# Kernel tuning notes

Hardware: AMD Instinct MI355X
Metric: run time of the kernel (lower is better)

The kernel has to match this reference:

```python
import jax, jax.numpy as jnp
import numpy as np

B, T, D, V, L, HM = 4, 2048, 128, 64, 12, 512
EPS = 1e-5
SCALE = float(np.sqrt(D))


def setup_inputs() -> dict:
    key = jax.random.key(0)
    ks = jax.random.split(key, 12)
    s = 0.02
    x = jax.random.randint(ks[0], (B, T), 0, V)
    pos_emb = jax.random.normal(ks[1], (T, D), jnp.float32) * s
    # per-layer params stacked on leading L axis; Linear weights in torch (out,in) layout
    Wq = jax.random.normal(ks[2], (L, D, D), jnp.float32) * s
    Wk = jax.random.normal(ks[3], (L, D, D), jnp.float32) * s
    Wv = jax.random.normal(ks[4], (L, D, D), jnp.float32) * s
    ln1_g = jnp.ones((L, D), jnp.float32)
    ln1_b = jnp.zeros((L, D), jnp.float32)
    W1 = jax.random.normal(ks[5], (L, HM, D), jnp.float32) * s
    b1 = jnp.zeros((L, HM), jnp.float32)
    W2 = jax.random.normal(ks[6], (L, D, HM), jnp.float32) * s
    b2 = jnp.zeros((L, D), jnp.float32)
    ln2_g = jnp.ones((L, D), jnp.float32)
    ln2_b = jnp.zeros((L, D), jnp.float32)
    Wro = jax.random.normal(ks[7], (1, D), jnp.float32) * s
    bro = jnp.zeros((1,), jnp.float32)
    return dict(x=x, pos_emb=pos_emb, Wq=Wq, Wk=Wk, Wv=Wv, ln1_g=ln1_g, ln1_b=ln1_b,
                W1=W1, b1=b1, W2=W2, b2=b2, ln2_g=ln2_g, ln2_b=ln2_b, Wro=Wro, bro=bro)


def _layernorm(h, g, b):
    mu = jnp.mean(h, axis=-1, keepdims=True)
    var = jnp.mean(jnp.square(h - mu), axis=-1, keepdims=True)
    return (h - mu) * jax.lax.rsqrt(var + EPS) * g + b


def _token_embeddings(x):
    # -(c - x)^2 / 2 over class ids, zero-padded up to D
    ar = jnp.arange(V, dtype=jnp.float32)  # [V]
    leave = -jnp.square(ar - x[..., None].astype(jnp.float32)) * 0.5  # [B,T,V]
    return jnp.pad(leave, ((0, 0), (0, 0), (0, D - V)))  # [B,T,D]


def _forward(x, pos_emb, Wq, Wk, Wv, ln1_g, ln1_b, W1, b1, W2, b2, ln2_g, ln2_b, Wro, bro):
    H = _token_embeddings(x) + pos_emb[None]  # [B,T,D]

    def step(Hc, p):
        wq, wk, wv, g1, be1, w1, bb1, w2, bb2, g2, be2 = p
        H1 = _layernorm(Hc, g1, be1)
        q = H1 @ wq.T
        k = H1 @ wk.T
        v = H1 @ wv.T
        scores = jnp.einsum('bid,bjd->bij', q, k) / SCALE  # [B,T,T]
        attn = jax.nn.softmax(scores, axis=-1)
        Hc = Hc + jnp.einsum('bij,bjd->bid', attn, v)
        H2 = _layernorm(Hc, g2, be2)
        Hc = Hc + (jax.nn.gelu(H2 @ w1.T + bb1, approximate=False) @ w2.T + bb2)
        return Hc, None

    H, _ = jax.lax.scan(step, H, (Wq, Wk, Wv, ln1_g, ln1_b, W1, b1, W2, b2, ln2_g, ln2_b))
    pred = H @ Wro.T + bro  # [B,T,1]
    return pred[:, :, 0]


def reference(x, pos_emb, Wq, Wk, Wv, ln1_g, ln1_b, W1, b1, W2, b2, ln2_g, ln2_b, Wro, bro):
    return _forward(x, pos_emb, Wq, Wk, Wv, ln1_g, ln1_b, W1, b1, W2, b2, ln2_g, ln2_b, Wro, bro)
```

## Files before the change

kernel.cpp:

```cpp
#include <hip/hip_runtime.h>
#include <math.h>

#define D 128
#define T 2048
#define BATCH 4
#define HMID 512
#define NLAYER 12

#define KSPLIT 8
#define KPB (T / KSPLIT)
#define BK 64

#if defined(__has_builtin)
#if __has_builtin(__builtin_amdgcn_global_load_lds)
#define USE_GLL 1
#endif
#endif
#ifndef USE_GLL
#define USE_GLL 0
#endif

typedef unsigned short u16;
typedef __attribute__((ext_vector_type(8))) short bf16x8;
typedef __attribute__((ext_vector_type(16))) float f32x16;

__device__ inline u16 f2bf(float x) {
    unsigned u = __builtin_bit_cast(unsigned, x);
    return (u16)((u + 0x7FFFu + ((u >> 16) & 1u)) >> 16);
}
__device__ inline float bf2f(u16 v) {
    return __builtin_bit_cast(float, (unsigned)v << 16);
}
__device__ inline unsigned pkt(float a, float b) {
    return (__builtin_bit_cast(unsigned, a) >> 16) |
           (__builtin_bit_cast(unsigned, b) & 0xFFFF0000u);
}

__device__ inline void ln_stats32(const float (*Ct)[133], float* mu_s, float* rs_s, int tid) {
    const int q = tid >> 3, e8 = tid & 7;
    float s = 0.f;
#pragma unroll
    for (int c = 0; c < 16; c++) s += Ct[q][e8 * 16 + c];
    s += __shfl_xor(s, 1); s += __shfl_xor(s, 2); s += __shfl_xor(s, 4);
    float mu = s * (1.f / D);
    float s2 = 0.f;
#pragma unroll
    for (int c = 0; c < 16; c++) {
        float d0 = Ct[q][e8 * 16 + c] - mu;
        s2 += d0 * d0;
    }
    s2 += __shfl_xor(s2, 1); s2 += __shfl_xor(s2, 2); s2 += __shfl_xor(s2, 4);
    if (e8 == 0) { mu_s[q] = mu; rs_s[q] = rsqrtf(s2 * (1.f / D) + 1e-5f); }
}

__device__ inline void build_as(const float (*Ct)[133], const float* mu_s, const float* rs_s,
                                const float* __restrict__ g, const float* __restrict__ bb,
                                u16* As, int tid) {
    const int row = tid >> 3, e8 = tid & 7;
    const float mu = mu_s[row], rs = rs_s[row];
#pragma unroll
    for (int cc = 0; cc < 2; cc++) {
        int c = e8 * 2 + cc;
        u16 tmp[8];
#pragma unroll
        for (int j = 0; j < 8; j++) {
            int d = c * 8 + j;
            tmp[j] = f2bf((Ct[row][d] - mu) * rs * g[d] + bb[d]);
        }
        *(uint4*)&As[((size_t)c * 32 + (row ^ (c & 7))) * 8] = *(uint4*)tmp;
    }
}

__device__ inline void stage_w(const u16* __restrict__ W, int ldw, u16* Wst, int tid) {
#pragma unroll
    for (int i = 0; i < 8; i++) {
        int ci = tid + 256 * i;
        int row = ci >> 4, c = ci & 15;
        *(uint4*)&Wst[((size_t)c * 128 + (row ^ c)) * 8] =
            *(const uint4*)(W + (size_t)row * ldw + c * 8);
    }
}

__device__ inline f32x16 mm_32x128(const u16* As, const u16* Wst, int wv, int ql, int h) {
    f32x16 a;
#pragma unroll
    for (int r = 0; r < 16; r++) a[r] = 0.f;
#pragma unroll
    for (int s = 0; s < 8; s++) {
        int ch = 2 * s + h;
        bf16x8 af = *(const bf16x8*)&As[((size_t)ch * 32 + (ql ^ (ch & 7))) * 8];
        bf16x8 bf = *(const bf16x8*)&Wst[((size_t)ch * 128 + ((wv * 32 + ql) ^ ch)) * 8];
        a = __builtin_amdgcn_mfma_f32_32x32x16_bf16(af, bf, a, 0, 0, 0);
    }
    return a;
}

__device__ inline void qkv_phase(const u16* As, const u16* __restrict__ Wqkvl, u16* Wst,
                                 u16* __restrict__ qb, u16* __restrict__ kb,
                                 u16* __restrict__ vt, int m0, int tid) {
    const int wv = tid >> 6, l = tid & 63, h = l >> 5, ql = l & 31;
    const int bbk = m0 >> 11;
    const int tl0 = m0 & 2047;
#pragma unroll
    for (int sl = 0; sl < 3; sl++) {
        __syncthreads();
        stage_w(Wqkvl + (size_t)sl * 128 * D, D, Wst, tid);
        __syncthreads();
        f32x16 a = mm_32x128(As, Wst, wv, ql, h);
        const int n = wv * 32 + ql;
        if (sl == 2) {
            u16* dst = vt + (size_t)bbk * D * T + (size_t)n * T + tl0;
#pragma unroll
            for (int g = 0; g < 4; g++) {
                ushort4 o;
                o.x = f2bf(a[4 * g + 0]);
                o.y = f2bf(a[4 * g + 1]);
                o.z = f2bf(a[4 * g + 2]);
                o.w = f2bf(a[4 * g + 3]);
                *(ushort4*)(dst + 8 * g + 4 * h) = o;
            }
        } else {
            u16* dst = (sl == 0) ? qb : kb;
#pragma unroll
            for (int r = 0; r < 16; r++) {
                int row = (r & 3) + 8 * (r >> 2) + 4 * h;
                dst[(size_t)(m0 + row) * D + n] = f2bf(a[r]);
            }
        }
    }
}

__global__ __launch_bounds__(256) void conv_all(const float* __restrict__ Wq,
                                                const float* __restrict__ Wk,
                                                const float* __restrict__ Wv,
                                                const float* __restrict__ W1,
                                                const float* __restrict__ W2,
                                                u16* __restrict__ Wqkv,
                                                u16* __restrict__ W1b,
                                                u16* __restrict__ W2b, float qscale) {
    const int NQ = NLAYER * 3 * D * D;
    const int NW = NLAYER * HMID * D;
    int idx = blockIdx.x * 256 + threadIdx.x;
    if (idx < NQ) {
        int lN = idx / (3 * D * D);
        int rem = idx - lN * (3 * D * D);
        int s = rem >> 14;
        int off = rem & 16383;
        const float* src = (s == 0) ? Wq : ((s == 1) ? Wk : Wv);
        Wqkv[idx] = f2bf(src[lN * 16384 + off] * ((s == 0) ? qscale : 1.f));
    } else if (idx < NQ + NW) {
        W1b[idx - NQ] = f2bf(W1[idx - NQ]);
    } else if (idx < NQ + 2 * NW) {
        W2b[idx - NQ - NW] = f2bf(W2[idx - NQ - NW]);
    }
}

__global__ __launch_bounds__(256, 1) void embed_qkv(const int* __restrict__ x,
                                                    const float* __restrict__ pos,
                                                    const float* __restrict__ g1,
                                                    const float* __restrict__ b1g,
                                                    const u16* __restrict__ Wqkv0,
                                                    u16* __restrict__ qb, u16* __restrict__ kb,
                                                    u16* __restrict__ vt,
                                                    float* __restrict__ H) {
    __shared__ float Ct[32][133];
    __shared__ float mu_s[32], rs_s[32];
    __shared__ u16 As[16 * 32 * 8];
    __shared__ u16 Wst[16 * 128 * 8];
    const int tid = threadIdx.x;
    const int m0 = blockIdx.x * 32;
    {
        const int d = tid & 127, rr = tid >> 7;
#pragma unroll
        for (int i = 0; i < 16; i++) {
            int row = rr * 16 + i;
            int tok = m0 + row;
            int t = tok & (T - 1);
            float e = 0.f;
            if (d < 64) {
                float diff = (float)d - (float)x[tok];
                e = -0.5f * diff * diff;
            }
            float v = e + pos[(size_t)t * D + d];
            Ct[row][d] = v;
            H[(size_t)tok * D + d] = v;
        }
    }
    __syncthreads();
    ln_stats32(Ct, mu_s, rs_s, tid);
    __syncthreads();
    build_as(Ct, mu_s, rs_s, g1, b1g, As, tid);
    qkv_phase(As, Wqkv0, Wst, qb, kb, vt, m0, tid);
}

__global__ __launch_bounds__(256, 2) void attn_mfma(const u16* __restrict__ qg,
                                                    const u16* __restrict__ kg,
                                                    const u16* __restrict__ vtg,
                                                    u16* __restrict__ Op,
                                                    float* __restrict__ ml) {
    __shared__ u16 Ks[64 * 128];
    __shared__ u16 Vt[128 * 64];
    const int tid = threadIdx.x;
    const int w = tid >> 6;
    const int l = tid & 63;
    const int h = l >> 5;
    const int ql = l & 31;
    const int qblk = blockIdx.x;
    const int ks = blockIdx.y;
    const int b = qblk >> 4;

    const size_t qrow = (size_t)qblk * 128 + w * 32 + ql;
    bf16x8 qf[8];
#pragma unroll
    for (int c = 0; c < 8; c++)
        qf[c] = *(const bf16x8*)(qg + qrow * D + c * 16 + h * 8);

    f32x16 ot[4];
#pragma unroll
    for (int t = 0; t < 4; t++)
#pragma unroll
        for (int r = 0; r < 16; r++) ot[t][r] = 0.f;
    float l_run = 0.f;

    const size_t kgb = (size_t)b * T * D;
    const size_t vtb = (size_t)b * D * T;

    for (int kt = 0; kt < KPB / BK; kt++) {
        const int kbase = ks * KPB + kt * BK;
        __syncthreads();
#if USE_GLL
#pragma unroll
        for (int i = 0; i < 4; i++) {
            int s = w * 256 + i * 64 + l;
            int row = s >> 4, ch = (s & 15) ^ (row & 7);
            __builtin_amdgcn_global_load_lds(
                (const __attribute__((address_space(1))) void*)(kg + kgb + (size_t)(kbase + row) * D + ch * 8),
                (__attribute__((address_space(3))) void*)&Ks[(w * 256 + i * 64) * 8], 16, 0, 0);
        }
#pragma unroll
        for (int i = 0; i < 4; i++) {
            int s = w * 256 + i * 64 + l;
            int dd = s >> 3, ch = (s & 7) ^ (dd & 7);
            __builtin_amdgcn_global_load_lds(
                (const __attribute__((address_space(1))) void*)(vtg + vtb + (size_t)dd * T + kbase + ch * 8),
                (__attribute__((address_space(3))) void*)&Vt[(w * 256 + i * 64) * 8], 16, 0, 0);
        }
#else
#pragma unroll
        for (int i = 0; i < 4; i++) {
            int s = tid + i * 256;
            int row = s >> 4, ch = (s & 15) ^ (row & 7);
            *(uint4*)&Ks[(size_t)s * 8] = *(const uint4*)(kg + kgb + (size_t)(kbase + row) * D + ch * 8);
            int dd = s >> 3, ch2 = (s & 7) ^ (dd & 7);
            *(uint4*)&Vt[(size_t)s * 8] = *(const uint4*)(vtg + vtb + (size_t)dd * T + kbase + ch2 * 8);
        }
#endif
        __syncthreads();
        f32x16 st0, st1;
#pragma unroll
        for (int r = 0; r < 16; r++) { st0[r] = 0.f; st1[r] = 0.f; }
#pragma unroll
        for (int c = 0; c < 8; c++) {
            int ch = c * 2 + h;
            bf16x8 k0 = *(const bf16x8*)&Ks[(ql * 16 + (ch ^ (ql & 7))) * 8];
            bf16x8 k1 = *(const bf16x8*)&Ks[((32 + ql) * 16 + (ch ^ (ql & 7))) * 8];
            st0 = __builtin_amdgcn_mfma_f32_32x32x16_bf16(k0, qf[c], st0, 0, 0, 0);
            st1 = __builtin_amdgcn_mfma_f32_32x32x16_bf16(k1, qf[c], st1, 0, 0, 0);
        }
        float rs = 0.f;
#pragma unroll
        for (int r = 0; r < 16; r++) {
            float p0 = exp2f(st0[r]); st0[r] = p0;
            float p1 = exp2f(st1[r]); st1[r] = p1;
            rs += p0 + p1;
        }
        rs += __shfl_xor(rs, 32);
        l_run += rs;
        uint2 pk0[4], pk1[4];
#pragma unroll
        for (int g = 0; g < 4; g++) {
            pk0[g].x = pkt(st0[4 * g + 0], st0[4 * g + 1]);
            pk0[g].y = pkt(st0[4 * g + 2], st0[4 * g + 3]);
            pk1[g].x = pkt(st1[4 * g + 0], st1[4 * g + 1]);
            pk1[g].y = pkt(st1[4 * g + 2], st1[4 * g + 3]);
        }
#pragma unroll
        for (int c = 0; c < 4; c++) {
            const uint2* pk = (c < 2) ? pk0 : pk1;
            const int cc = c & 1;
            uint2 own = h ? pk[2 * cc + 1] : pk[2 * cc];
            uint2 snd = h ? pk[2 * cc] : pk[2 * cc + 1];
            uint2 rcv;
            rcv.x = (unsigned)__shfl_xor((int)snd.x, 32);
            rcv.y = (unsigned)__shfl_xor((int)snd.y, 32);
            uint4 fr;
            fr.x = h ? rcv.x : own.x;
            fr.y = h ? rcv.y : own.y;
            fr.z = h ? own.x : rcv.x;
            fr.w = h ? own.y : rcv.y;
            bf16x8 pf = __builtin_bit_cast(bf16x8, fr);
            int ch = c * 2 + h;
#pragma unroll
            for (int t = 0; t < 4; t++) {
                bf16x8 vf = *(const bf16x8*)&Vt[((t * 32 + ql) * 8 + (ch ^ (ql & 7))) * 8];
                ot[t] = __builtin_amdgcn_mfma_f32_32x32x16_bf16(vf, pf, ot[t], 0, 0, 0);
            }
        }
    }
    size_t base = (((size_t)(qblk * KSPLIT + ks)) * 4 + w) * (128 * 32);
#pragma unroll
    for (int t = 0; t < 4; t++)
#pragma unroll
        for (int r = 0; r < 16; r++) {
            int dd = (r & 3) + 8 * (r >> 2) + 4 * h + 32 * t;
            Op[base + (size_t)dd * 32 + ql] = f2bf(ot[t][r]);
        }
    if (h == 0) {
        int qi = w * 32 + ql;
        ml[(size_t)(qblk * KSPLIT + ks) * 256 + qi] = 0.f;
        ml[(size_t)(qblk * KSPLIT + ks) * 256 + 128 + qi] = l_run;
    }
}

template <int LAST>
__global__ __launch_bounds__(256, 1) void layer_tail(
    const u16* __restrict__ Op, const float* __restrict__ ml,
    float* __restrict__ H,
    const float* __restrict__ g2, const float* __restrict__ b2l,
    const u16* __restrict__ W1l, const float* __restrict__ b1l,
    const u16* __restrict__ W2l, const float* __restrict__ b2bias,
    const float* __restrict__ g1n, const float* __restrict__ b1n,
    const u16* __restrict__ Wqkvn,
    u16* __restrict__ qb, u16* __restrict__ kb, u16* __restrict__ vt,
    const float* __restrict__ Wro, const float* __restrict__ bro,
    float* __restrict__ outp) {
    __shared__ float Ct[32][133];
    __shared__ float mu_s[32], rs_s[32];
    __shared__ u16 As[16 * 32 * 8];
    __shared__ u16 midS[64 * 32 * 8];
    __shared__ u16 Wst[16 * 128 * 8];

    const int tid = threadIdx.x;
    const int bid = blockIdx.x;
    const int qblk = bid >> 2;
    const int wq = bid & 3;
    const int m0 = bid * 32;
    const int wv = tid >> 6;
    const int l = tid & 63;
    const int h = l >> 5;
    const int ql = l & 31;

    {
        const int dg = tid >> 5;
        float m[KSPLIT], lv[KSPLIT];
        float M = -1e30f;
#pragma unroll
        for (int ks = 0; ks < KSPLIT; ks++) {
            m[ks] = ml[(size_t)(qblk * KSPLIT + ks) * 256 + wq * 32 + ql];
            lv[ks] = ml[(size_t)(qblk * KSPLIT + ks) * 256 + 128 + wq * 32 + ql];
            M = fmaxf(M, m[ks]);
        }
        float L = 0.f, f[KSPLIT];
#pragma unroll
        for (int ks = 0; ks < KSPLIT; ks++) { f[ks] = exp2f(m[ks] - M); L += lv[ks] * f[ks]; }
        float invL = 1.f / L;
        float acc[16];
#pragma unroll
        for (int i = 0; i < 16; i++) acc[i] = 0.f;
#pragma unroll
        for (int ks = 0; ks < KSPLIT; ks++) {
            size_t base = (((size_t)(qblk * KSPLIT + ks)) * 4 + wq) * (128 * 32);
#pragma unroll
            for (int i = 0; i < 16; i++)
                acc[i] += bf2f(Op[base + (size_t)(dg * 16 + i) * 32 + ql]) * f[ks];
        }
#pragma unroll
        for (int i = 0; i < 16; i++) Ct[ql][dg * 16 + i] = acc[i] * invL;
    }
    __syncthreads();
    {
        const int d = tid & 127, rr = tid >> 7;
#pragma unroll
        for (int i = 0; i < 16; i++) {
            int row = rr * 16 + i;
            Ct[row][d] += H[(size_t)(m0 + row) * D + d];
        }
    }
    __syncthreads();
    ln_stats32(Ct, mu_s, rs_s, tid);
    __syncthreads();
    build_as(Ct, mu_s, rs_s, g2, b2l, As, tid);
#pragma unroll
    for (int nc = 0; nc < 4; nc++) {
        __syncthreads();
        stage_w(W1l + (size_t)nc * 128 * D, D, Wst, tid);
        __syncthreads();
        f32x16 a = mm_32x128(As, Wst, wv, ql, h);
        const int n = nc * 128 + wv * 32 + ql;
        const int ch2 = n >> 3, sub = n & 7;
        const float bv = b1l[n];
#pragma unroll
        for (int r = 0; r < 16; r++) {
            int row = (r & 3) + 8 * (r >> 2) + 4 * h;
            float v = a[r] + bv;
            v = 0.5f * v * (1.f + erff(v * 0.7071067811865475f));
            midS[((size_t)ch2 * 32 + (row ^ (ch2 & 7))) * 8 + sub] = f2bf(v);
        }
    }
    f32x16 a2;
#pragma unroll
    for (int r = 0; r < 16; r++) a2[r] = 0.f;
#pragma unroll
    for (int kc = 0; kc < 4; kc++) {
        __syncthreads();
        stage_w(W2l + (size_t)kc * 128, HMID, Wst, tid);
        __syncthreads();
#pragma unroll
        for (int s = 0; s < 8; s++) {
            int ch = 2 * s + h;
            int gch = kc * 16 + ch;
            bf16x8 af = *(const bf16x8*)&midS[((size_t)gch * 32 + (ql ^ (gch & 7))) * 8];
            bf16x8 bf = *(const bf16x8*)&Wst[((size_t)ch * 128 + ((wv * 32 + ql) ^ ch)) * 8];
            a2 = __builtin_amdgcn_mfma_f32_32x32x16_bf16(af, bf, a2, 0, 0, 0);
        }
    }
    {
        const int col = wv * 32 + ql;
        const float bv = b2bias[col];
#pragma unroll
        for (int r = 0; r < 16; r++) {
            int row = (r & 3) + 8 * (r >> 2) + 4 * h;
            float v = a2[r] + bv + Ct[row][col];
            Ct[row][col] = v;
            H[(size_t)(m0 + row) * D + col] = v;
        }
    }
    __syncthreads();
    if (LAST) {
        const int q = tid >> 3, e8 = tid & 7;
        float s = 0.f;
#pragma unroll
        for (int c = 0; c < 16; c++) s += Ct[q][e8 * 16 + c] * Wro[e8 * 16 + c];
        s += __shfl_xor(s, 1); s += __shfl_xor(s, 2); s += __shfl_xor(s, 4);
        if (e8 == 0) outp[m0 + q] = s + bro[0];
    } else {
        ln_stats32(Ct, mu_s, rs_s, tid);
        __syncthreads();
        build_as(Ct, mu_s, rs_s, g1n, b1n, As, tid);
        qkv_phase(As, Wqkvn, Wst, qb, kb, vt, m0, tid);
    }
}

extern "C" void kernel_launch(void* const* d_in, const int* in_sizes, int n_in,
                              void* d_out, int out_size, void* d_ws, size_t ws_size,
                              hipStream_t stream) {
    const int* x = (const int*)d_in[0];
    const float* pos = (const float*)d_in[1];
    const float* Wq = (const float*)d_in[2];
    const float* Wk = (const float*)d_in[3];
    const float* Wv = (const float*)d_in[4];
    const float* ln1g = (const float*)d_in[5];
    const float* ln1b = (const float*)d_in[6];
    const float* W1 = (const float*)d_in[7];
    const float* b1 = (const float*)d_in[8];
    const float* W2 = (const float*)d_in[9];
    const float* b2 = (const float*)d_in[10];
    const float* ln2g = (const float*)d_in[11];
    const float* ln2b = (const float*)d_in[12];
    const float* Wro = (const float*)d_in[13];
    const float* bro = (const float*)d_in[14];
    float* out = (float*)d_out;

    const size_t NTOK = (size_t)BATCH * T;
    const size_t HSZ = NTOK * D;
    float* ws = (float*)d_ws;
    float* H = ws;
    u16* qb = (u16*)(ws + HSZ);
    u16* kb = (u16*)(ws + HSZ + HSZ / 2);
    u16* vt = (u16*)(ws + 2 * HSZ);
    u16* Op = (u16*)(ws + 2 * HSZ + HSZ / 2);
    float* mlbuf = ws + 7 * HSZ;
    u16* Wqkv = (u16*)(ws + 7 * HSZ + 131072);
    u16* W1b = Wqkv + (size_t)NLAYER * 3 * D * D;
    u16* W2b = W1b + (size_t)NLAYER * HMID * D;

    const float qscale = 1.4426950408889634f / 11.313708498984761f;

    conv_all<<<dim3(8448), 256, 0, stream>>>(Wq, Wk, Wv, W1, W2, Wqkv, W1b, W2b, qscale);
    embed_qkv<<<dim3(256), 256, 0, stream>>>(x, pos, ln1g, ln1b, Wqkv, qb, kb, vt, H);

    for (int lay = 0; lay < NLAYER; lay++) {
        attn_mfma<<<dim3(64, KSPLIT), 256, 0, stream>>>(qb, kb, vt, Op, mlbuf);
        if (lay < NLAYER - 1) {
            layer_tail<0><<<dim3(256), 256, 0, stream>>>(
                Op, mlbuf, H,
                ln2g + (size_t)lay * D, ln2b + (size_t)lay * D,
                W1b + (size_t)lay * HMID * D, b1 + (size_t)lay * HMID,
                W2b + (size_t)lay * D * HMID, b2 + (size_t)lay * D,
                ln1g + (size_t)(lay + 1) * D, ln1b + (size_t)(lay + 1) * D,
                Wqkv + (size_t)(lay + 1) * 3 * D * D,
                qb, kb, vt, Wro, bro, nullptr);
        } else {
            layer_tail<1><<<dim3(256), 256, 0, stream>>>(
                Op, mlbuf, H,
                ln2g + (size_t)lay * D, ln2b + (size_t)lay * D,
                W1b + (size_t)lay * HMID * D, b1 + (size_t)lay * HMID,
                W2b + (size_t)lay * D * HMID, b2 + (size_t)lay * D,
                ln1g, ln1b, Wqkv,
                qb, kb, vt, Wro, bro, out);
        }
    }
}
```

Baseline: 607.9 us.

## Fuse attention with layer tail into one kernel per layer using double-buffered QKV

Replaces the split-K attention kernel plus separate tail kernel with a single fused_layer kernel. Each 256-thread block handles 32 queries and splits the full 2048-key range across its four waves, then reduces the partial outputs and row sums in shared memory instead of writing Op and ml to global memory. The next layer's q/k/v go into a separate ping-pong buffer to avoid read/write races. The grid shrinks to 256 blocks, each with a long serial key loop, so parallelism drops (previously 512 attention blocks), and the MLP loop is reordered to interleave W1/W2 chunks in less shared memory.

```diff
diff --git a/kernel.cpp b/kernel.cpp
--- a/kernel.cpp
+++ b/kernel.cpp
@@ -6,10 +6,6 @@
 #define BATCH 4
 #define HMID 512
 #define NLAYER 12
-
-#define KSPLIT 8
-#define KPB (T / KSPLIT)
-#define BK 64
 
 #if defined(__has_builtin)
 #if __has_builtin(__builtin_amdgcn_global_load_lds)
@@ -36,7 +32,7 @@
            (__builtin_bit_cast(unsigned, b) & 0xFFFF0000u);
 }
 
-__device__ inline void ln_stats32(const float (*Ct)[133], float* mu_s, float* rs_s, int tid) {
+__device__ inline void ln_stats32(const float (*Ct)[132], float* mu_s, float* rs_s, int tid) {
     const int q = tid >> 3, e8 = tid & 7;
     float s = 0.f;
 #pragma unroll
@@ -53,7 +49,7 @@
     if (e8 == 0) { mu_s[q] = mu; rs_s[q] = rsqrtf(s2 * (1.f / D) + 1e-5f); }
 }
 
-__device__ inline void build_as(const float (*Ct)[133], const float* mu_s, const float* rs_s,
+__device__ inline void build_as(const float (*Ct)[132], const float* mu_s, const float* rs_s,
                                 const float* __restrict__ g, const float* __restrict__ bb,
                                 u16* As, int tid) {
     const int row = tid >> 3, e8 = tid & 7;
@@ -100,7 +96,7 @@
                                  u16* __restrict__ vt, int m0, int tid) {
     const int wv = tid >> 6, l = tid & 63, h = l >> 5, ql = l & 31;
     const int bbk = m0 >> 11;
-    const int tl0 = m0 & 2047;
+    const int tl0 = m0 & (T - 1);
 #pragma unroll
     for (int sl = 0; sl < 3; sl++) {
         __syncthreads();
@@ -163,7 +159,7 @@
                                                     u16* __restrict__ qb, u16* __restrict__ kb,
                                                     u16* __restrict__ vt,
                                                     float* __restrict__ H) {
-    __shared__ float Ct[32][133];
+    __shared__ float Ct[32][132];
     __shared__ float mu_s[32], rs_s[32];
     __shared__ u16 As[16 * 32 * 8];
     __shared__ u16 Wst[16 * 128 * 8];
@@ -193,27 +189,47 @@
     qkv_phase(As, Wqkv0, Wst, qb, kb, vt, m0, tid);
 }
 
-__global__ __launch_bounds__(256, 2) void attn_mfma(const u16* __restrict__ qg,
-                                                    const u16* __restrict__ kg,
-                                                    const u16* __restrict__ vtg,
-                                                    u16* __restrict__ Op,
-                                                    float* __restrict__ ml) {
-    __shared__ u16 Ks[64 * 128];
-    __shared__ u16 Vt[128 * 64];
+template <int LAST>
+__global__ __launch_bounds__(256, 2) void fused_layer(
+    const u16* __restrict__ qg, const u16* __restrict__ kg, const u16* __restrict__ vtg,
+    float* __restrict__ H,
+    const float* __restrict__ g2, const float* __restrict__ b2l,
+    const u16* __restrict__ W1l, const float* __restrict__ b1l,
+    const u16* __restrict__ W2l, const float* __restrict__ b2bias,
+    const float* __restrict__ g1n, const float* __restrict__ b1n,
+    const u16* __restrict__ Wqkvn,
+    u16* __restrict__ qbn, u16* __restrict__ kbn, u16* __restrict__ vtn,
+    const float* __restrict__ Wro, const float* __restrict__ bro,
+    float* __restrict__ outp) {
+    __shared__ union {
+        struct { u16 Kt[128 * 16 * 8]; u16 Vt[128 * 16 * 8]; } at;
+        struct {
+            float Ct[32][132];
+            union {
+                u16 Ob[4][128 * 32];
+                struct { u16 As[16 * 32 * 8]; u16 midS[16 * 32 * 8]; u16 Wst[16 * 128 * 8]; } tl;
+            } u2;
+        } t;
+    } sm;
+    __shared__ float lstat[4][32];
+    __shared__ float mu_s[32], rs_s[32];
+
     const int tid = threadIdx.x;
+    const int bid = blockIdx.x;
+    const int bq = bid & 3;
+    const int m0 = bq * T + (bid >> 2) * 32;
     const int w = tid >> 6;
     const int l = tid & 63;
     const int h = l >> 5;
     const int ql = l & 31;
-    const int qblk = blockIdx.x;
-    const int ks = blockIdx.y;
-    const int b = qblk >> 4;
-
-    const size_t qrow = (size_t)qblk * 128 + w * 32 + ql;
+
+    const u16* kgb = kg + (size_t)bq * T * D;
+    const u16* vtb = vtg + (size_t)bq * D * T;
+
     bf16x8 qf[8];
 #pragma unroll
     for (int c = 0; c < 8; c++)
-        qf[c] = *(const bf16x8*)(qg + qrow * D + c * 16 + h * 8);
+        qf[c] = *(const bf16x8*)(qg + (size_t)(m0 + ql) * D + c * 16 + h * 8);
 
     f32x16 ot[4];
 #pragma unroll
@@ -222,72 +238,66 @@
         for (int r = 0; r < 16; r++) ot[t][r] = 0.f;
     float l_run = 0.f;
 
-    const size_t kgb = (size_t)b * T * D;
-    const size_t vtb = (size_t)b * D * T;
-
-    for (int kt = 0; kt < KPB / BK; kt++) {
-        const int kbase = ks * KPB + kt * BK;
+    for (int kt = 0; kt < 16; kt++) {
+        const int kbase = kt * 128;
         __syncthreads();
 #if USE_GLL
 #pragma unroll
-        for (int i = 0; i < 4; i++) {
-            int s = w * 256 + i * 64 + l;
-            int row = s >> 4, ch = (s & 15) ^ (row & 7);
+        for (int i = 0; i < 8; i++) {
+            int ci = w * 64 + 256 * i + l;
+            int row = ci >> 4, ch = (ci & 15) ^ (row & 7);
             __builtin_amdgcn_global_load_lds(
-                (const __attribute__((address_space(1))) void*)(kg + kgb + (size_t)(kbase + row) * D + ch * 8),
-                (__attribute__((address_space(3))) void*)&Ks[(w * 256 + i * 64) * 8], 16, 0, 0);
-        }
-#pragma unroll
-        for (int i = 0; i < 4; i++) {
-            int s = w * 256 + i * 64 + l;
-            int dd = s >> 3, ch = (s & 7) ^ (dd & 7);
+                (const __attribute__((address_space(1))) void*)(kgb + (size_t)(kbase + row) * D + ch * 8),
+                (__attribute__((address_space(3))) void*)&sm.at.Kt[(w * 64 + 256 * i) * 8], 16, 0, 0);
+        }
+#pragma unroll
+        for (int i = 0; i < 8; i++) {
+            int ci = w * 64 + 256 * i + l;
+            int dd = ci >> 4, ch = (ci & 15) ^ (dd & 7);
             __builtin_amdgcn_global_load_lds(
-                (const __attribute__((address_space(1))) void*)(vtg + vtb + (size_t)dd * T + kbase + ch * 8),
-                (__attribute__((address_space(3))) void*)&Vt[(w * 256 + i * 64) * 8], 16, 0, 0);
+                (const __attribute__((address_space(1))) void*)(vtb + (size_t)dd * T + kbase + ch * 8),
+                (__attribute__((address_space(3))) void*)&sm.at.Vt[(w * 64 + 256 * i) * 8], 16, 0, 0);
         }
 #else
 #pragma unroll
-        for (int i = 0; i < 4; i++) {
-            int s = tid + i * 256;
-            int row = s >> 4, ch = (s & 15) ^ (row & 7);
-            *(uint4*)&Ks[(size_t)s * 8] = *(const uint4*)(kg + kgb + (size_t)(kbase + row) * D + ch * 8);
-            int dd = s >> 3, ch2 = (s & 7) ^ (dd & 7);
-            *(uint4*)&Vt[(size_t)s * 8] = *(const uint4*)(vtg + vtb + (size_t)dd * T + kbase + ch2 * 8);
+        for (int i = 0; i < 8; i++) {
+            int ci = tid + 256 * i;
+            int row = ci >> 4, ch = (ci & 15) ^ (row & 7);
+            *(uint4*)&sm.at.Kt[(size_t)ci * 8] =
+                *(const uint4*)(kgb + (size_t)(kbase + row) * D + ch * 8);
+            int ch2 = (ci & 15) ^ (row & 7);
+            *(uint4*)&sm.at.Vt[(size_t)ci * 8] =
+                *(const uint4*)(vtb + (size_t)row * T + kbase + ch2 * 8);
         }
 #endif
         __syncthreads();
-        f32x16 st0, st1;
-#pragma unroll
-        for (int r = 0; r < 16; r++) { st0[r] = 0.f; st1[r] = 0.f; }
+        const int krow = w * 32 + ql;
+        f32x16 st;
+#pragma unroll
+        for (int r = 0; r < 16; r++) st[r] = 0.f;
 #pragma unroll
         for (int c = 0; c < 8; c++) {
-            int ch = c * 2 + h;
-            bf16x8 k0 = *(const bf16x8*)&Ks[(ql * 16 + (ch ^ (ql & 7))) * 8];
-            bf16x8 k1 = *(const bf16x8*)&Ks[((32 + ql) * 16 + (ch ^ (ql & 7))) * 8];
-            st0 = __builtin_amdgcn_mfma_f32_32x32x16_bf16(k0, qf[c], st0, 0, 0, 0);
-            st1 = __builtin_amdgcn_mfma_f32_32x32x16_bf16(k1, qf[c], st1, 0, 0, 0);
+            int ch = 2 * c + h;
+            bf16x8 kf = *(const bf16x8*)&sm.at.Kt[((size_t)krow * 16 + (ch ^ (krow & 7))) * 8];
+            st = __builtin_amdgcn_mfma_f32_32x32x16_bf16(kf, qf[c], st, 0, 0, 0);
         }
         float rs = 0.f;
 #pragma unroll
         for (int r = 0; r < 16; r++) {
-            float p0 = exp2f(st0[r]); st0[r] = p0;
-            float p1 = exp2f(st1[r]); st1[r] = p1;
-            rs += p0 + p1;
+            float p = exp2f(st[r]);
+            st[r] = p;
+            rs += p;
         }
         rs += __shfl_xor(rs, 32);
         l_run += rs;
-        uint2 pk0[4], pk1[4];
+        uint2 pk[4];
 #pragma unroll
         for (int g = 0; g < 4; g++) {
-            pk0[g].x = pkt(st0[4 * g + 0], st0[4 * g + 1]);
-            pk0[g].y = pkt(st0[4 * g + 2], st0[4 * g + 3]);
-            pk1[g].x = pkt(st1[4 * g + 0], st1[4 * g + 1]);
-            pk1[g].y = pkt(st1[4 * g + 2], st1[4 * g + 3]);
-        }
-#pragma unroll
-        for (int c = 0; c < 4; c++) {
-            const uint2* pk = (c < 2) ? pk0 : pk1;
-            const int cc = c & 1;
+            pk[g].x = pkt(st[4 * g + 0], st[4 * g + 1]);
+            pk[g].y = pkt(st[4 * g + 2], st[4 * g + 3]);
+        }
+#pragma unroll
+        for (int cc = 0; cc < 2; cc++) {
             uint2 own = h ? pk[2 * cc + 1] : pk[2 * cc];
             uint2 snd = h ? pk[2 * cc] : pk[2 * cc + 1];
             uint2 rcv;
@@ -299,139 +309,82 @@
             fr.z = h ? own.x : rcv.x;
             fr.w = h ? own.y : rcv.y;
             bf16x8 pf = __builtin_bit_cast(bf16x8, fr);
-            int ch = c * 2 + h;
+            const int kch = w * 4 + cc * 2 + h;
 #pragma unroll
             for (int t = 0; t < 4; t++) {
-                bf16x8 vf = *(const bf16x8*)&Vt[((t * 32 + ql) * 8 + (ch ^ (ql & 7))) * 8];
+                int drow = t * 32 + ql;
+                bf16x8 vf = *(const bf16x8*)&sm.at.Vt[((size_t)drow * 16 + (kch ^ (drow & 7))) * 8];
                 ot[t] = __builtin_amdgcn_mfma_f32_32x32x16_bf16(vf, pf, ot[t], 0, 0, 0);
             }
         }
     }
-    size_t base = (((size_t)(qblk * KSPLIT + ks)) * 4 + w) * (128 * 32);
-#pragma unroll
-    for (int t = 0; t < 4; t++)
-#pragma unroll
-        for (int r = 0; r < 16; r++) {
-            int dd = (r & 3) + 8 * (r >> 2) + 4 * h + 32 * t;
-            Op[base + (size_t)dd * 32 + ql] = f2bf(ot[t][r]);
-        }
-    if (h == 0) {
-        int qi = w * 32 + ql;
-        ml[(size_t)(qblk * KSPLIT + ks) * 256 + qi] = 0.f;
-        ml[(size_t)(qblk * KSPLIT + ks) * 256 + 128 + qi] = l_run;
-    }
-}
-
-template <int LAST>
-__global__ __launch_bounds__(256, 1) void layer_tail(
-    const u16* __restrict__ Op, const float* __restrict__ ml,
-    float* __restrict__ H,
-    const float* __restrict__ g2, const float* __restrict__ b2l,
-    const u16* __restrict__ W1l, const float* __restrict__ b1l,
-    const u16* __restrict__ W2l, const float* __restrict__ b2bias,
-    const float* __restrict__ g1n, const float* __restrict__ b1n,
-    const u16* __restrict__ Wqkvn,
-    u16* __restrict__ qb, u16* __restrict__ kb, u16* __restrict__ vt,
-    const float* __restrict__ Wro, const float* __restrict__ bro,
-    float* __restrict__ outp) {
-    __shared__ float Ct[32][133];
-    __shared__ float mu_s[32], rs_s[32];
-    __shared__ u16 As[16 * 32 * 8];
-    __shared__ u16 midS[64 * 32 * 8];
-    __shared__ u16 Wst[16 * 128 * 8];
-
-    const int tid = threadIdx.x;
-    const int bid = blockIdx.x;
-    const int qblk = bid >> 2;
-    const int wq = bid & 3;
-    const int m0 = bid * 32;
-    const int wv = tid >> 6;
-    const int l = tid & 63;
-    const int h = l >> 5;
-    const int ql = l & 31;
-
+    __syncthreads();
     {
-        const int dg = tid >> 5;
-        float m[KSPLIT], lv[KSPLIT];
-        float M = -1e30f;
-#pragma unroll
-        for (int ks = 0; ks < KSPLIT; ks++) {
-            m[ks] = ml[(size_t)(qblk * KSPLIT + ks) * 256 + wq * 32 + ql];
-            lv[ks] = ml[(size_t)(qblk * KSPLIT + ks) * 256 + 128 + wq * 32 + ql];
-            M = fmaxf(M, m[ks]);
-        }
-        float L = 0.f, f[KSPLIT];
-#pragma unroll
-        for (int ks = 0; ks < KSPLIT; ks++) { f[ks] = exp2f(m[ks] - M); L += lv[ks] * f[ks]; }
+        u16* Ob = sm.t.u2.Ob[w];
+#pragma unroll
+        for (int t = 0; t < 4; t++)
+#pragma unroll
+            for (int r = 0; r < 16; r++) {
+                int dd = (r & 3) + 8 * (r >> 2) + 4 * h + 32 * t;
+                Ob[dd * 32 + ql] = f2bf(ot[t][r]);
+            }
+        if (h == 0) lstat[w][ql] = l_run;
+    }
+    __syncthreads();
+    {
+        const int q2 = tid & 31, dg = tid >> 5;
+        float L = lstat[0][q2] + lstat[1][q2] + lstat[2][q2] + lstat[3][q2];
         float invL = 1.f / L;
-        float acc[16];
-#pragma unroll
-        for (int i = 0; i < 16; i++) acc[i] = 0.f;
-#pragma unroll
-        for (int ks = 0; ks < KSPLIT; ks++) {
-            size_t base = (((size_t)(qblk * KSPLIT + ks)) * 4 + wq) * (128 * 32);
-#pragma unroll
-            for (int i = 0; i < 16; i++)
-                acc[i] += bf2f(Op[base + (size_t)(dg * 16 + i) * 32 + ql]) * f[ks];
-        }
-#pragma unroll
-        for (int i = 0; i < 16; i++) Ct[ql][dg * 16 + i] = acc[i] * invL;
-    }
-    __syncthreads();
-    {
-        const int d = tid & 127, rr = tid >> 7;
 #pragma unroll
         for (int i = 0; i < 16; i++) {
-            int row = rr * 16 + i;
-            Ct[row][d] += H[(size_t)(m0 + row) * D + d];
-        }
-    }
-    __syncthreads();
-    ln_stats32(Ct, mu_s, rs_s, tid);
-    __syncthreads();
-    build_as(Ct, mu_s, rs_s, g2, b2l, As, tid);
-#pragma unroll
-    for (int nc = 0; nc < 4; nc++) {
-        __syncthreads();
-        stage_w(W1l + (size_t)nc * 128 * D, D, Wst, tid);
-        __syncthreads();
-        f32x16 a = mm_32x128(As, Wst, wv, ql, h);
-        const int n = nc * 128 + wv * 32 + ql;
-        const int ch2 = n >> 3, sub = n & 7;
-        const float bv = b1l[n];
+            int d = dg * 16 + i;
+            float s = bf2f(sm.t.u2.Ob[0][d * 32 + q2]) + bf2f(sm.t.u2.Ob[1][d * 32 + q2]) +
+                      bf2f(sm.t.u2.Ob[2][d * 32 + q2]) + bf2f(sm.t.u2.Ob[3][d * 32 + q2]);
+            sm.t.Ct[q2][d] = s * invL + H[(size_t)(m0 + q2) * D + d];
+        }
+    }
+    __syncthreads();
+    ln_stats32(sm.t.Ct, mu_s, rs_s, tid);
+    __syncthreads();
+    build_as(sm.t.Ct, mu_s, rs_s, g2, b2l, sm.t.u2.tl.As, tid);
+    f32x16 a2;
+#pragma unroll
+    for (int r = 0; r < 16; r++) a2[r] = 0.f;
+    for (int kc = 0; kc < 4; kc++) {
+        __syncthreads();
+        stage_w(W1l + (size_t)kc * 128 * D, D, sm.t.u2.tl.Wst, tid);
+        __syncthreads();
+        f32x16 a = mm_32x128(sm.t.u2.tl.As, sm.t.u2.tl.Wst, w, ql, h);
+        const int nl = w * 32 + ql;
+        const int ch2 = nl >> 3, sub = nl & 7;
+        const float bv = b1l[kc * 128 + nl];
 #pragma unroll
         for (int r = 0; r < 16; r++) {
             int row = (r & 3) + 8 * (r >> 2) + 4 * h;
             float v = a[r] + bv;
             v = 0.5f * v * (1.f + erff(v * 0.7071067811865475f));
-            midS[((size_t)ch2 * 32 + (row ^ (ch2 & 7))) * 8 + sub] = f2bf(v);
-        }
-    }
-    f32x16 a2;
-#pragma unroll
-    for (int r = 0; r < 16; r++) a2[r] = 0.f;
-#pragma unroll
-    for (int kc = 0; kc < 4; kc++) {
-        __syncthreads();
-        stage_w(W2l + (size_t)kc * 128, HMID, Wst, tid);
+            sm.t.u2.tl.midS[((size_t)ch2 * 32 + (row ^ (ch2 & 7))) * 8 + sub] = f2bf(v);
+        }
+        __syncthreads();
+        stage_w(W2l + (size_t)kc * 128, HMID, sm.t.u2.tl.Wst, tid);
         __syncthreads();
 #pragma unroll
         for (int s = 0; s < 8; s++) {
             int ch = 2 * s + h;
-            int gch = kc * 16 + ch;
-            bf16x8 af = *(const bf16x8*)&midS[((size_t)gch * 32 + (ql ^ (gch & 7))) * 8];
-            bf16x8 bf = *(const bf16x8*)&Wst[((size_t)ch * 128 + ((wv * 32 + ql) ^ ch)) * 8];
+            bf16x8 af = *(const bf16x8*)&sm.t.u2.tl.midS[((size_t)ch * 32 + (ql ^ (ch & 7))) * 8];
+            bf16x8 bf = *(const bf16x8*)&sm.t.u2.tl.Wst[((size_t)ch * 128 + ((w * 32 + ql) ^ ch)) * 8];
             a2 = __builtin_amdgcn_mfma_f32_32x32x16_bf16(af, bf, a2, 0, 0, 0);
         }
     }
+    __syncthreads();
     {
-        const int col = wv * 32 + ql;
+        const int col = w * 32 + ql;
         const float bv = b2bias[col];
 #pragma unroll
         for (int r = 0; r < 16; r++) {
             int row = (r & 3) + 8 * (r >> 2) + 4 * h;
-            float v = a2[r] + bv + Ct[row][col];
-            Ct[row][col] = v;
+            float v = a2[r] + bv + sm.t.Ct[row][col];
+            sm.t.Ct[row][col] = v;
             H[(size_t)(m0 + row) * D + col] = v;
         }
     }
@@ -440,14 +393,14 @@
         const int q = tid >> 3, e8 = tid & 7;
         float s = 0.f;
 #pragma unroll
-        for (int c = 0; c < 16; c++) s += Ct[q][e8 * 16 + c] * Wro[e8 * 16 + c];
+        for (int c = 0; c < 16; c++) s += sm.t.Ct[q][e8 * 16 + c] * Wro[e8 * 16 + c];
         s += __shfl_xor(s, 1); s += __shfl_xor(s, 2); s += __shfl_xor(s, 4);
         if (e8 == 0) outp[m0 + q] = s + bro[0];
     } else {
-        ln_stats32(Ct, mu_s, rs_s, tid);
-        __syncthreads();
-        build_as(Ct, mu_s, rs_s, g1n, b1n, As, tid);
-        qkv_phase(As, Wqkvn, Wst, qb, kb, vt, m0, tid);
+        ln_stats32(sm.t.Ct, mu_s, rs_s, tid);
+        __syncthreads();
+        build_as(sm.t.Ct, mu_s, rs_s, g1n, b1n, sm.t.u2.tl.As, tid);
+        qkv_phase(sm.t.u2.tl.As, Wqkvn, sm.t.u2.tl.Wst, qbn, kbn, vtn, m0, tid);
     }
 }
 
@@ -475,39 +428,45 @@
     const size_t HSZ = NTOK * D;
     float* ws = (float*)d_ws;
     float* H = ws;
-    u16* qb = (u16*)(ws + HSZ);
-    u16* kb = (u16*)(ws + HSZ + HSZ / 2);
-    u16* vt = (u16*)(ws + 2 * HSZ);
-    u16* Op = (u16*)(ws + 2 * HSZ + HSZ / 2);
-    float* mlbuf = ws + 7 * HSZ;
-    u16* Wqkv = (u16*)(ws + 7 * HSZ + 131072);
+    u16* qb0 = (u16*)(ws + HSZ);
+    u16* kb0 = qb0 + HSZ;
+    u16* vt0 = kb0 + HSZ;
+    u16* qb1 = vt0 + HSZ;
+    u16* kb1 = qb1 + HSZ;
+    u16* vt1 = kb1 + HSZ;
+    u16* Wqkv = vt1 + HSZ;
     u16* W1b = Wqkv + (size_t)NLAYER * 3 * D * D;
     u16* W2b = W1b + (size_t)NLAYER * HMID * D;
 
     const float qscale = 1.4426950408889634f / 11.313708498984761f;
 
     conv_all<<<dim3(8448), 256, 0, stream>>>(Wq, Wk, Wv, W1, W2, Wqkv, W1b, W2b, qscale);
-    embed_qkv<<<dim3(256), 256, 0, stream>>>(x, pos, ln1g, ln1b, Wqkv, qb, kb, vt, H);
+    embed_qkv<<<dim3(256), 256, 0, stream>>>(x, pos, ln1g, ln1b, Wqkv, qb0, kb0, vt0, H);
 
     for (int lay = 0; lay < NLAYER; lay++) {
-        attn_mfma<<<dim3(64, KSPLIT), 256, 0, stream>>>(qb, kb, vt, Op, mlbuf);
+        u16* qc = (lay & 1) ? qb1 : qb0;
+        u16* kc = (lay & 1) ? kb1 : kb0;
+        u16* vc = (lay & 1) ? vt1 : vt0;
+        u16* qn = (lay & 1) ? qb0 : qb1;
+        u16* kn = (lay & 1) ? kb0 : kb1;
+        u16* vn = (lay & 1) ? vt0 : vt1;
         if (lay < NLAYER - 1) {
-            layer_tail<0><<<dim3(256), 256, 0, stream>>>(
-                Op, mlbuf, H,
+            fused_layer<0><<<dim3(256), 256, 0, stream>>>(
+                qc, kc, vc, H,
                 ln2g + (size_t)lay * D, ln2b + (size_t)lay * D,
                 W1b + (size_t)lay * HMID * D, b1 + (size_t)lay * HMID,
                 W2b + (size_t)lay * D * HMID, b2 + (size_t)lay * D,
                 ln1g + (size_t)(lay + 1) * D, ln1b + (size_t)(lay + 1) * D,
                 Wqkv + (size_t)(lay + 1) * 3 * D * D,
-                qb, kb, vt, Wro, bro, nullptr);
+                qn, kn, vn, Wro, bro, nullptr);
         } else {
-            layer_tail<1><<<dim3(256), 256, 0, stream>>>(
-                Op, mlbuf, H,
+            fused_layer<1><<<dim3(256), 256, 0, stream>>>(
+                qc, kc, vc, H,
                 ln2g + (size_t)lay * D, ln2b + (size_t)lay * D,
                 W1b + (size_t)lay * HMID * D, b1 + (size_t)lay * HMID,
                 W2b + (size_t)lay * D * HMID, b2 + (size_t)lay * D,
                 ln1g, ln1b, Wqkv,
-                qb, kb, vt, Wro, bro, out);
-        }
-    }
-}
+                qn, kn, vn, Wro, bro, out);
+        }
+    }
+}
```

Result: slower. 816.8 us (+34.4%).
